# Kernel tuning notes

Measured on AMD Instinct MI355X. Metric: run time of the kernel, lower is better.

The kernel has to match this reference:

```python
import math
import jax, jax.numpy as jnp
import numpy as np

S, H, E = 8192, 4096, 64          # tokens, hidden, experts
CAPACITY_FACTOR = 1.0
MIN_CAPACITY = 4


def setup_inputs() -> dict:
    key = jax.random.key(0)
    k1, k2 = jax.random.split(key)
    return {
        "gate_input": jax.random.normal(k1, (S, H), dtype=jnp.float32),
        "gate_weight": jax.random.normal(k2, (E, H), dtype=jnp.float32) * 0.02,
    }


def reference(gate_input, gate_weight):
    # Router projection (always fp32, bias-free Linear)
    logits = gate_input.astype(jnp.float32) @ gate_weight.astype(jnp.float32).T  # [S, E]
    gates = jax.nn.softmax(logits, axis=1)
    s, e = gates.shape
    # _capacity with capacity_factor*2 for top-2; static given shapes
    capacity = max(int(math.ceil(s * (CAPACITY_FACTOR * 2.0) / e)), MIN_CAPACITY)

    # top-2 expert selection
    _, sel = jax.lax.top_k(gates, 2)                       # [S, 2]
    mask1 = jax.nn.one_hot(sel[:, 0], e, dtype=jnp.int32)  # [S, E]
    mask2 = jax.nn.one_hot(sel[:, 1], e, dtype=jnp.int32)

    # cumsum-based slot assignment within each expert
    loc1 = jnp.cumsum(mask1, axis=0) - 1
    loc2 = jnp.cumsum(mask2, axis=0) - 1 + jnp.sum(mask1, axis=0, keepdims=True)

    # aux load-balancing loss (aux_loss_coef = 0 -> no gate rescale)
    me = jnp.mean(gates, axis=0)
    ce = jnp.mean(mask1.astype(jnp.float32), axis=0)
    l_aux = jnp.mean(me * ce) * e * e

    # drop tokens over capacity
    mask1 = mask1 * (loc1 < capacity).astype(jnp.int32)
    mask2 = mask2 * (loc2 < capacity).astype(jnp.int32)
    idx_in_exp1 = jnp.sum(loc1 * mask1, axis=1)            # [S]
    idx_in_exp2 = jnp.sum(loc2 * mask2, axis=1)

    m1f = mask1.astype(jnp.float32)
    m2f = mask2.astype(jnp.float32)
    w1 = jnp.max(gates * m1f, axis=1)
    w2 = jnp.max(gates * m2f, axis=1)
    denom = jnp.maximum(w1 + w2, jnp.finfo(jnp.float32).eps)
    w1 = w1 / denom
    w2 = w2 / denom

    gates1 = w1[:, None] * m1f                             # [S, E]
    gates2 = w2[:, None] * m2f
    loc1_sc = jax.nn.one_hot(idx_in_exp1, capacity, dtype=jnp.float32)  # [S, C]
    loc2_sc = jax.nn.one_hot(idx_in_exp2, capacity, dtype=jnp.float32)
    combine_weights = (gates1[:, :, None] * loc1_sc[:, None, :]
                       + gates2[:, :, None] * loc2_sc[:, None, :])      # [S, E, C]
    dispatch_mask = combine_weights > 0
    return l_aux, combine_weights, dispatch_mask
```

## Files before the change

kernel.cpp:

```cpp
#include <hip/hip_runtime.h>
#include <cstdint>
#include <cstddef>

constexpr int S = 8192;
constexpr int H = 4096;
constexpr int E = 64;
constexpr int CAP = 256;
constexpr int KSPLIT = 4;
constexpr int KCHUNK = H / KSPLIT;
constexpr int BK = 32;
constexpr int BM = 64;
constexpr long long SEC = (long long)S * E * CAP;
constexpr long long OUTN = 2 * SEC + 1;
constexpr int F4_PER_BLOCK = 131072;
constexpr int F4_PER_ITER = 16;

typedef float f4_t __attribute__((ext_vector_type(4)));

__global__ __launch_bounds__(256)
void k_gemm_fill(const float* __restrict__ A, const float* __restrict__ W,
                 float* __restrict__ part, float* __restrict__ out) {
    __shared__ float As[BK][BM + 4];
    __shared__ float Bs[BK][E + 4];
    const int tid = threadIdx.x;
    const int m0 = blockIdx.x * BM;
    const int kbase = blockIdx.y * KCHUNK;
    const int b = blockIdx.y * gridDim.x + blockIdx.x;
    const int lr = tid >> 3;
    const int lc = (tid & 7) << 2;
    const int ty = tid >> 4;
    const int tx = tid & 15;

    f4_t* __restrict__ fill = (f4_t*)out + (size_t)b * F4_PER_BLOCK + tid;
    const f4_t z4 = {0.f, 0.f, 0.f, 0.f};

    float acc[4][4];
#pragma unroll
    for (int i = 0; i < 4; ++i)
#pragma unroll
        for (int j = 0; j < 4; ++j) acc[i][j] = 0.f;

    for (int it = 0; it < KCHUNK / BK; ++it) {
        const int kc = it * BK;
        const float* ap = A + (size_t)(m0 + lr) * H + (kbase + kc + lc);
        const float4 av0 = *(const float4*)ap;
        const float4 av1 = *(const float4*)(ap + (size_t)32 * H);
        const float* bp = W + (size_t)lr * H + (kbase + kc + lc);
        const float4 bv0 = *(const float4*)bp;
        const float4 bv1 = *(const float4*)(bp + (size_t)32 * H);
        __syncthreads();
        As[lc + 0][lr] = av0.x; As[lc + 1][lr] = av0.y;
        As[lc + 2][lr] = av0.z; As[lc + 3][lr] = av0.w;
        As[lc + 0][lr + 32] = av1.x; As[lc + 1][lr + 32] = av1.y;
        As[lc + 2][lr + 32] = av1.z; As[lc + 3][lr + 32] = av1.w;
        Bs[lc + 0][lr] = bv0.x; Bs[lc + 1][lr] = bv0.y;
        Bs[lc + 2][lr] = bv0.z; Bs[lc + 3][lr] = bv0.w;
        Bs[lc + 0][lr + 32] = bv1.x; Bs[lc + 1][lr + 32] = bv1.y;
        Bs[lc + 2][lr + 32] = bv1.z; Bs[lc + 3][lr + 32] = bv1.w;
        __syncthreads();
        f4_t* d = fill + (size_t)it * (F4_PER_ITER * 256);
#pragma unroll
        for (int j = 0; j < F4_PER_ITER; ++j)
            __builtin_nontemporal_store(z4, d + j * 256);
#pragma unroll
        for (int kk = 0; kk < BK; ++kk) {
            const float4 a = *(const float4*)&As[kk][ty * 4];
            const float4 bb = *(const float4*)&Bs[kk][tx * 4];
            acc[0][0] = fmaf(a.x, bb.x, acc[0][0]);
            acc[0][1] = fmaf(a.x, bb.y, acc[0][1]);
            acc[0][2] = fmaf(a.x, bb.z, acc[0][2]);
            acc[0][3] = fmaf(a.x, bb.w, acc[0][3]);
            acc[1][0] = fmaf(a.y, bb.x, acc[1][0]);
            acc[1][1] = fmaf(a.y, bb.y, acc[1][1]);
            acc[1][2] = fmaf(a.y, bb.z, acc[1][2]);
            acc[1][3] = fmaf(a.y, bb.w, acc[1][3]);
            acc[2][0] = fmaf(a.z, bb.x, acc[2][0]);
            acc[2][1] = fmaf(a.z, bb.y, acc[2][1]);
            acc[2][2] = fmaf(a.z, bb.z, acc[2][2]);
            acc[2][3] = fmaf(a.z, bb.w, acc[2][3]);
            acc[3][0] = fmaf(a.w, bb.x, acc[3][0]);
            acc[3][1] = fmaf(a.w, bb.y, acc[3][1]);
            acc[3][2] = fmaf(a.w, bb.z, acc[3][2]);
            acc[3][3] = fmaf(a.w, bb.w, acc[3][3]);
        }
    }
    if (b == 0 && tid == 0) out[(size_t)OUTN - 1] = 0.f;
    float* P = part + (size_t)blockIdx.y * S * E;
#pragma unroll
    for (int i = 0; i < 4; ++i) {
        float4 v = make_float4(acc[i][0], acc[i][1], acc[i][2], acc[i][3]);
        *(float4*)&P[(size_t)(m0 + ty * 4 + i) * E + tx * 4] = v;
    }
}

__global__ __launch_bounds__(256)
void k_router(const float* __restrict__ part, int* __restrict__ e1a,
              int* __restrict__ e2a, float* __restrict__ g1a,
              float* __restrict__ g2a, float* __restrict__ sumg,
              int* __restrict__ cnt1) {
    const int lane = threadIdx.x & 63;
    const int gw = blockIdx.x * 4 + (threadIdx.x >> 6);
    float lsum = 0.f;
    int lcnt = 0;
    for (int s = gw; s < S; s += 256) {
        const float* p = part + (size_t)s * E + lane;
        float l = p[0] + p[(size_t)S * E] + p[2 * (size_t)S * E]
                + p[3 * (size_t)S * E];
        float m = l;
#pragma unroll
        for (int o = 32; o; o >>= 1) m = fmaxf(m, __shfl_xor(m, o));
        const float ex = __expf(l - m);
        float Z = ex;
#pragma unroll
        for (int o = 32; o; o >>= 1) Z += __shfl_xor(Z, o);
        const float g = ex / Z;
        lsum += g;
        float v1 = g; int i1 = lane;
#pragma unroll
        for (int o = 32; o; o >>= 1) {
            const float ov = __shfl_xor(v1, o);
            const int oi = __shfl_xor(i1, o);
            if (ov > v1 || (ov == v1 && oi < i1)) { v1 = ov; i1 = oi; }
        }
        float v2 = (lane == i1) ? -1.f : g; int i2 = lane;
#pragma unroll
        for (int o = 32; o; o >>= 1) {
            const float ov = __shfl_xor(v2, o);
            const int oi = __shfl_xor(i2, o);
            if (ov > v2 || (ov == v2 && oi < i2)) { v2 = ov; i2 = oi; }
        }
        if (i1 == lane) lcnt++;
        if (lane == 0) {
            e1a[s] = i1; e2a[s] = i2; g1a[s] = v1; g2a[s] = v2;
        }
    }
    atomicAdd(&sumg[lane], lsum);
    atomicAdd(&cnt1[lane], lcnt);
}

__global__ __launch_bounds__(64)
void k_assign(const int* __restrict__ e1a, const int* __restrict__ e2a,
              int* __restrict__ slot1a, int* __restrict__ slot2a) {
    const int e = blockIdx.x;
    const int lane = threadIdx.x;
    const unsigned long long below = (1ull << lane) - 1ull;
    int cnt = 0;
    for (int c = 0; c < S; c += 64) {
        const int s = c + lane;
        const bool m = (e1a[s] == e);
        const unsigned long long bal = __ballot(m);
        if (m) {
            const int rank = cnt + __popcll(bal & below);
            slot1a[s] = (rank < CAP) ? rank : -1;
        }
        cnt += __popcll(bal);
    }
    const int total1 = cnt;
    int cnt2 = 0;
    for (int c = 0; c < S; c += 64) {
        const int s = c + lane;
        const bool m = (e2a[s] == e);
        const unsigned long long bal = __ballot(m);
        if (m) {
            const int rank = total1 + cnt2 + __popcll(bal & below);
            slot2a[s] = (rank < CAP) ? rank : -1;
        }
        cnt2 += __popcll(bal);
    }
}

__global__ __launch_bounds__(256)
void k_scatter(const int* __restrict__ e1a, const int* __restrict__ e2a,
               const float* __restrict__ g1a, const float* __restrict__ g2a,
               const int* __restrict__ slot1a, const int* __restrict__ slot2a,
               const float* __restrict__ sumg, const int* __restrict__ cnt1,
               float* __restrict__ out) {
    const int s = blockIdx.x * 256 + threadIdx.x;
    float* comb = out + 1;
    float* mask = out + 1 + (size_t)SEC;
    const int sl1 = slot1a[s], sl2 = slot2a[s];
    const float w1 = (sl1 >= 0) ? g1a[s] : 0.f;
    const float w2 = (sl2 >= 0) ? g2a[s] : 0.f;
    const float denom = fmaxf(w1 + w2, 1.1920928955078125e-07f);
    if (sl1 >= 0) {
        const size_t off = ((size_t)s * E + e1a[s]) * CAP + sl1;
        comb[off] = w1 / denom;
        mask[off] = 1.f;
    }
    if (sl2 >= 0) {
        const size_t off = ((size_t)s * E + e2a[s]) * CAP + sl2;
        comb[off] = w2 / denom;
        mask[off] = 1.f;
    }
    if (blockIdx.x == 0 && threadIdx.x < 64) {
        const int lane = threadIdx.x;
        float v = sumg[lane] * (float)cnt1[lane];
#pragma unroll
        for (int o = 32; o; o >>= 1) v += __shfl_xor(v, o);
        if (lane == 0) out[0] = v * (float)E / ((float)S * (float)S);
    }
}

extern "C" void kernel_launch(void* const* d_in, const int* in_sizes, int n_in,
                              void* d_out, int out_size, void* d_ws,
                              size_t ws_size, hipStream_t stream) {
    const float* A = (const float*)d_in[0];
    const float* W = (const float*)d_in[1];
    float* out = (float*)d_out;

    char* ws = (char*)d_ws;
    float* part = (float*)ws;
    size_t off = (size_t)KSPLIT * S * E * sizeof(float);
    int* e1a = (int*)(ws + off);      off += (size_t)S * 4;
    int* e2a = (int*)(ws + off);      off += (size_t)S * 4;
    float* g1a = (float*)(ws + off);  off += (size_t)S * 4;
    float* g2a = (float*)(ws + off);  off += (size_t)S * 4;
    int* slot1a = (int*)(ws + off);   off += (size_t)S * 4;
    int* slot2a = (int*)(ws + off);   off += (size_t)S * 4;
    float* sumg = (float*)(ws + off); off += (size_t)E * 4;
    int* cnt1 = (int*)(ws + off);     off += (size_t)E * 4;

    hipMemsetAsync(sumg, 0, 2 * (size_t)E * 4, stream);

    k_gemm_fill<<<dim3(S / BM, KSPLIT), 256, 0, stream>>>(A, W, part, out);
    k_router<<<64, 256, 0, stream>>>(part, e1a, e2a, g1a, g2a, sumg, cnt1);
    k_assign<<<E, 64, 0, stream>>>(e1a, e2a, slot1a, slot2a);
    k_scatter<<<S / 256, 256, 0, stream>>>(e1a, e2a, g1a, g2a, slot1a, slot2a,
                                           sumg, cnt1, out);
}
```

Before: 1.319 ms.

## Split zero-fill into dedicated blocks of a combined GEMM/fill grid

Rather than interleaving non-temporal zero stores of the huge output inside each GEMM k-loop iteration, the kernel now launches a 1D grid in which the first 512 blocks do the split-K router GEMM and 2048 extra blocks only zero-fill the output. The hipMemsetAsync for the sumg/cnt1 accumulators is removed and folded into the last fill block, saving a separate launch. The goal is to let fill-only blocks saturate write bandwidth independently of the compute blocks. The risk is that the GEMM blocks no longer hide the fill behind their own memory traffic, and that scheduling of the extra blocks becomes the limiting factor.

```diff
diff --git a/kernel.cpp b/kernel.cpp
--- a/kernel.cpp
+++ b/kernel.cpp
@@ -12,36 +12,52 @@
 constexpr int BM = 64;
 constexpr long long SEC = (long long)S * E * CAP;
 constexpr long long OUTN = 2 * SEC + 1;
-constexpr int F4_PER_BLOCK = 131072;
-constexpr int F4_PER_ITER = 16;
+constexpr int NGEMM = (S / BM) * KSPLIT;
+constexpr int NFILL = 2048;
+constexpr int F4_PER_FILL_BLOCK = 32768;
 
 typedef float f4_t __attribute__((ext_vector_type(4)));
 
 __global__ __launch_bounds__(256)
-void k_gemm_fill(const float* __restrict__ A, const float* __restrict__ W,
-                 float* __restrict__ part, float* __restrict__ out) {
+void k_main(const float* __restrict__ A, const float* __restrict__ W,
+            float* __restrict__ part, float* __restrict__ out,
+            float* __restrict__ sumg, int* __restrict__ cnt1) {
     __shared__ float As[BK][BM + 4];
     __shared__ float Bs[BK][E + 4];
+    const int b = blockIdx.x;
     const int tid = threadIdx.x;
-    const int m0 = blockIdx.x * BM;
-    const int kbase = blockIdx.y * KCHUNK;
-    const int b = blockIdx.y * gridDim.x + blockIdx.x;
+
+    if (b >= NGEMM) {
+        const int fb = b - NGEMM;
+        f4_t* __restrict__ dst =
+            (f4_t*)out + (size_t)fb * F4_PER_FILL_BLOCK + tid;
+        const f4_t z4 = {0.f, 0.f, 0.f, 0.f};
+#pragma unroll
+        for (int j = 0; j < F4_PER_FILL_BLOCK / 256; ++j)
+            __builtin_nontemporal_store(z4, dst + j * 256);
+        if (fb == NFILL - 1) {
+            if (tid == 0) out[(size_t)OUTN - 1] = 0.f;
+            if (tid < E) sumg[tid] = 0.f;
+            else if (tid < 2 * E) cnt1[tid - E] = 0;
+        }
+        return;
+    }
+
+    const int m0 = (b & (S / BM - 1)) * BM;
+    const int kb = b >> 7;
+    const int kbase = kb * KCHUNK;
     const int lr = tid >> 3;
     const int lc = (tid & 7) << 2;
     const int ty = tid >> 4;
     const int tx = tid & 15;
 
-    f4_t* __restrict__ fill = (f4_t*)out + (size_t)b * F4_PER_BLOCK + tid;
-    const f4_t z4 = {0.f, 0.f, 0.f, 0.f};
-
     float acc[4][4];
 #pragma unroll
     for (int i = 0; i < 4; ++i)
 #pragma unroll
         for (int j = 0; j < 4; ++j) acc[i][j] = 0.f;
 
-    for (int it = 0; it < KCHUNK / BK; ++it) {
-        const int kc = it * BK;
+    for (int kc = 0; kc < KCHUNK; kc += BK) {
         const float* ap = A + (size_t)(m0 + lr) * H + (kbase + kc + lc);
         const float4 av0 = *(const float4*)ap;
         const float4 av1 = *(const float4*)(ap + (size_t)32 * H);
@@ -58,10 +74,6 @@
         Bs[lc + 0][lr + 32] = bv1.x; Bs[lc + 1][lr + 32] = bv1.y;
         Bs[lc + 2][lr + 32] = bv1.z; Bs[lc + 3][lr + 32] = bv1.w;
         __syncthreads();
-        f4_t* d = fill + (size_t)it * (F4_PER_ITER * 256);
-#pragma unroll
-        for (int j = 0; j < F4_PER_ITER; ++j)
-            __builtin_nontemporal_store(z4, d + j * 256);
 #pragma unroll
         for (int kk = 0; kk < BK; ++kk) {
             const float4 a = *(const float4*)&As[kk][ty * 4];
@@ -84,8 +96,7 @@
             acc[3][3] = fmaf(a.w, bb.w, acc[3][3]);
         }
     }
-    if (b == 0 && tid == 0) out[(size_t)OUTN - 1] = 0.f;
-    float* P = part + (size_t)blockIdx.y * S * E;
+    float* P = part + (size_t)kb * S * E;
 #pragma unroll
     for (int i = 0; i < 4; ++i) {
         float4 v = make_float4(acc[i][0], acc[i][1], acc[i][2], acc[i][3]);
@@ -220,9 +231,7 @@
     float* sumg = (float*)(ws + off); off += (size_t)E * 4;
     int* cnt1 = (int*)(ws + off);     off += (size_t)E * 4;
 
-    hipMemsetAsync(sumg, 0, 2 * (size_t)E * 4, stream);
-
-    k_gemm_fill<<<dim3(S / BM, KSPLIT), 256, 0, stream>>>(A, W, part, out);
+    k_main<<<NGEMM + NFILL, 256, 0, stream>>>(A, W, part, out, sumg, cnt1);
     k_router<<<64, 256, 0, stream>>>(part, e1a, e2a, g1a, g2a, sumg, cnt1);
     k_assign<<<E, 64, 0, stream>>>(e1a, e2a, slot1a, slot2a);
     k_scatter<<<S / 256, 256, 0, stream>>>(e1a, e2a, g1a, g2a, slot1a, slot2a,
```

After: 1.296 ms. Within noise of the previous version (-1.7%).
